# Optimization experiments

Measured on AMD Instinct MI355X. Metric: run time of the kernel, lower is better.

Reference implementation:

```python
import jax, jax.numpy as jnp
import numpy as np

B, N, NPOINT, NSAMPLE = 8, 8192, 2048, 64
RADIUS = 0.2
C_IN = 64  # input feature channels; mlp[0]=64 -> 67 after use_xyz concat


def setup_inputs() -> dict:
    key = jax.random.key(0)
    ks = jax.random.split(key, 12)
    xyz = jax.random.uniform(ks[0], (B, N, 3), dtype=jnp.float32)
    features = jax.random.normal(ks[1], (B, N, C_IN), dtype=jnp.float32)
    inds = jax.random.randint(ks[2], (B, NPOINT), 0, N, dtype=jnp.int32)

    def mkw(k, cin, cout):
        return jax.random.normal(k, (cin, cout), jnp.float32) * (1.0 / np.sqrt(cin).astype(np.float32))

    w0 = mkw(ks[3], C_IN + 3, 64)
    w1 = mkw(ks[4], 64, 64)
    w2 = mkw(ks[5], 64, 128)
    # BN (inference) folded into per-channel scale/shift
    s0 = 1.0 + 0.1 * jax.random.normal(ks[6], (64,), jnp.float32)
    t0 = 0.1 * jax.random.normal(ks[7], (64,), jnp.float32)
    s1 = 1.0 + 0.1 * jax.random.normal(ks[8], (64,), jnp.float32)
    t1 = 0.1 * jax.random.normal(ks[9], (64,), jnp.float32)
    s2 = 1.0 + 0.1 * jax.random.normal(ks[10], (128,), jnp.float32)
    t2 = 0.1 * jax.random.normal(ks[11], (128,), jnp.float32)
    return dict(xyz=xyz, features=features, inds=inds,
                w0=w0, s0=s0, t0=t0, w1=w1, s1=s1, t1=t1, w2=w2, s2=s2, t2=t2)


def _ball_query(xyz, new_xyz):
    """First NSAMPLE point indices within RADIUS of each query; pad by repeating
    the first hit (matches CUDA ball_query semantics). xyz:(B,N,3) new_xyz:(B,S,3)."""
    nn = jnp.sum(xyz * xyz, axis=-1)            # (B,N)
    qq = jnp.sum(new_xyz * new_xyz, axis=-1)    # (B,S)
    d2 = qq[:, :, None] + nn[:, None, :] - 2.0 * jnp.einsum('bsc,bnc->bsn', new_xyz, xyz)
    within = d2 < (RADIUS * RADIUS)
    ar = jnp.arange(N, dtype=jnp.int32)
    keyed = jnp.where(within, ar[None, None, :], N)   # out-of-radius -> sentinel N
    keyed = jnp.sort(keyed, axis=-1)[:, :, :NSAMPLE]  # first hits in point order
    idx = jnp.where(keyed == N, keyed[:, :, :1], keyed)
    return jnp.minimum(idx, N - 1)


_gather = jax.vmap(lambda pts, i: pts[i])  # (N,C),(M,) -> (M,C) per batch


def reference(xyz, features, inds, w0, s0, t0, w1, s1, t1, w2, s2, t2):
    new_xyz = _gather(xyz, inds)                              # (B,S,3)
    idx = _ball_query(xyz, new_xyz)                           # (B,S,ns)
    flat = idx.reshape(B, NPOINT * NSAMPLE)
    g_xyz = _gather(xyz, flat).reshape(B, NPOINT, NSAMPLE, 3)
    g_xyz = (g_xyz - new_xyz[:, :, None, :]) / RADIUS         # normalize_xyz
    g_feat = _gather(features, flat).reshape(B, NPOINT, NSAMPLE, C_IN)
    x = jnp.concatenate([g_xyz, g_feat], axis=-1)             # (B,S,ns,C+3)
    for wgt, s, t in ((w0, s0, t0), (w1, s1, t1), (w2, s2, t2)):
        x = jax.nn.relu(jnp.einsum('bpsc,cd->bpsd', x, wgt) * s + t)
    new_features = jnp.max(x, axis=2)                         # max-pool over nsample
    return new_xyz, new_features, inds, idx
```

## Files before the change

### kernel.cpp

```cpp
#include <hip/hip_runtime.h>

#define BB 8
#define NN 8192
#define NPOINT 2048
#define NSAMPLE 64
#define CIN 64
#define RADIUS 0.2f
#define R2 (RADIUS * RADIUS)

#define OFF_NEWXYZ 0
#define OFF_FEAT (BB * NPOINT * 3)
#define OFF_INDS (OFF_FEAT + BB * NPOINT * 128)
#define OFF_IDX (OFF_INDS + BB * NPOINT)

typedef _Float16 half8 __attribute__((ext_vector_type(8)));
typedef _Float16 half4 __attribute__((ext_vector_type(4)));
typedef __fp16 f16x2 __attribute__((ext_vector_type(2)));
typedef float floatx16 __attribute__((ext_vector_type(16)));

#define P0 88
#define P1 72
#define X_LOC 0
#define H_LOC (64 * P0)
#define XH_WAVE (64 * P0 + 64 * P1)
#define WT0_S 0
#define WT1_S (64 * P0)
#define WT2_S (64 * P0 + 64 * P1)

#define QPW 8

__global__ __launch_bounds__(256) void ballq_kernel(
    const float* __restrict__ xyz, const int* __restrict__ inds,
    float* __restrict__ out) {
  __shared__ int sidx[4][2][NSAMPLE];
  const int wave = (blockIdx.x * 256 + threadIdx.x) >> 6;
  const int lane = threadIdx.x & 63;
  const int wid = threadIdx.x >> 6;
  const int q0 = wave * 2, q1 = q0 + 1;
  const int b = q0 >> 11;

  const float* xb = xyz + (size_t)b * NN * 3;
  const int i0 = inds[q0], i1 = inds[q1];
  const float c0x = xb[i0 * 3 + 0], c0y = xb[i0 * 3 + 1], c0z = xb[i0 * 3 + 2];
  const float c1x = xb[i1 * 3 + 0], c1y = xb[i1 * 3 + 1], c1z = xb[i1 * 3 + 2];

  if (lane < 2) {
    const int qq_ = lane ? q1 : q0;
    const int ii = lane ? i1 : i0;
    out[OFF_NEWXYZ + (size_t)qq_ * 3 + 0] = lane ? c1x : c0x;
    out[OFF_NEWXYZ + (size_t)qq_ * 3 + 1] = lane ? c1y : c0y;
    out[OFF_NEWXYZ + (size_t)qq_ * 3 + 2] = lane ? c1z : c0z;
    out[OFF_INDS + qq_] = (float)ii;
  }

  const float qq0 = c0x * c0x + c0y * c0y + c0z * c0z;
  const float qq1 = c1x * c1x + c1y * c1y + c1z * c1z;

  int cnt0 = 0, cnt1 = 0;
  float ax[4], ay[4], az[4];
#pragma unroll
  for (int k = 0; k < 4; ++k) {
    const float* p = xb + (size_t)(k * 64 + lane) * 3;
    ax[k] = p[0];
    ay[k] = p[1];
    az[k] = p[2];
  }
  for (int j0 = 0; j0 < NN; j0 += 256) {
    float bx[4] = {0}, by[4] = {0}, bz[4] = {0};
    const int jn = j0 + 256;
    if (jn < NN) {
#pragma unroll
      for (int k = 0; k < 4; ++k) {
        const float* p = xb + (size_t)(jn + k * 64 + lane) * 3;
        bx[k] = p[0];
        by[k] = p[1];
        bz[k] = p[2];
      }
    }
#pragma unroll
    for (int k = 0; k < 4; ++k) {
      const int j = j0 + k * 64 + lane;
      const float nn_ = ax[k] * ax[k] + ay[k] * ay[k] + az[k] * az[k];
      const float dot0 = c0x * ax[k] + c0y * ay[k] + c0z * az[k];
      const float dot1 = c1x * ax[k] + c1y * ay[k] + c1z * az[k];
      const bool hit0 = (qq0 + nn_ - 2.0f * dot0) < R2;
      const bool hit1 = (qq1 + nn_ - 2.0f * dot1) < R2;
      const unsigned long long m0 = __ballot(hit0);
      const unsigned long long m1 = __ballot(hit1);
      if (hit0) {
        const int pos = cnt0 + (int)__popcll(m0 & ((1ull << lane) - 1ull));
        if (pos < NSAMPLE) sidx[wid][0][pos] = j;
      }
      if (hit1) {
        const int pos = cnt1 + (int)__popcll(m1 & ((1ull << lane) - 1ull));
        if (pos < NSAMPLE) sidx[wid][1][pos] = j;
      }
      cnt0 += (int)__popcll(m0);
      cnt1 += (int)__popcll(m1);
    }
    if (cnt0 >= NSAMPLE && cnt1 >= NSAMPLE) break;
#pragma unroll
    for (int k = 0; k < 4; ++k) {
      ax[k] = bx[k];
      ay[k] = by[k];
      az[k] = bz[k];
    }
  }
  const int v0 = sidx[wid][0][lane < cnt0 ? lane : 0];
  out[OFF_IDX + (size_t)q0 * NSAMPLE + lane] = (float)v0;
  const int v1 = sidx[wid][1][lane < cnt1 ? lane : 0];
  out[OFF_IDX + (size_t)q1 * NSAMPLE + lane] = (float)v1;
}

__global__ __launch_bounds__(128, 2) void mlp_mfma(
    const float* __restrict__ xyz, const float* __restrict__ features,
    const int* __restrict__ inds,
    const float* __restrict__ w0, const float* __restrict__ s0,
    const float* __restrict__ t0, const float* __restrict__ w1,
    const float* __restrict__ s1, const float* __restrict__ t1,
    const float* __restrict__ w2, const float* __restrict__ s2,
    const float* __restrict__ t2, float* __restrict__ out) {
  __shared__ _Float16 sm[2 * XH_WAVE];
  const int tid = threadIdx.x;
  const int w = tid >> 6;
  const int l = tid & 63;
  const int l31 = l & 31;
  const int h5 = l >> 5;
  const int koff = h5 * 8;

  {
    const int d = tid >> 1, hf = tid & 1;
    const float sd0 = s0[d], td0 = t0[d], sd1 = s1[d];
#pragma unroll
    for (int j = 0; j < 44; ++j) {
      const int c = hf * 44 + j;
      float v = 0.0f;
      if (c < 64) v = w0[(3 + c) * 64 + d] * sd0;
      else if (c < 67) v = w0[(c - 64) * 64 + d] * sd0;
      else if (c == 67) v = td0;
      sm[WT0_S + d * P0 + c] = (_Float16)v;
    }
#pragma unroll
    for (int j = 0; j < 32; ++j) {
      const int c = hf * 32 + j;
      sm[WT1_S + d * P1 + c] = (_Float16)(w1[c * 64 + d] * sd1);
    }
    const int ch = tid;
    const float sch = s2[ch];
#pragma unroll
    for (int c = 0; c < 64; ++c)
      sm[WT2_S + ch * P1 + c] = (_Float16)(w2[c * 128 + ch] * sch);
  }
  __syncthreads();

  half8 b0f[2][5], b1f[2][4], b2f[4][4];
#pragma unroll
  for (int nt = 0; nt < 2; ++nt)
#pragma unroll
    for (int ks = 0; ks < 5; ++ks)
      b0f[nt][ks] =
          *(const half8*)&sm[WT0_S + (nt * 32 + l31) * P0 + ks * 16 + koff];
#pragma unroll
  for (int nt = 0; nt < 2; ++nt)
#pragma unroll
    for (int ks = 0; ks < 4; ++ks)
      b1f[nt][ks] =
          *(const half8*)&sm[WT1_S + (nt * 32 + l31) * P1 + ks * 16 + koff];
#pragma unroll
  for (int ct = 0; ct < 4; ++ct)
#pragma unroll
    for (int ks = 0; ks < 4; ++ks)
      b2f[ct][ks] =
          *(const half8*)&sm[WT2_S + (ct * 32 + l31) * P1 + ks * 16 + koff];
  const float t1v0 = t1[l31];
  const float t1v1 = t1[32 + l31];
  float t2v[4];
#pragma unroll
  for (int ct = 0; ct < 4; ++ct) t2v[ct] = t2[ct * 32 + l31];
  __syncthreads();

  _Float16* xbuf = sm + w * XH_WAVE + X_LOC;
  _Float16* hbuf = sm + w * XH_WAVE + H_LOC;
  {
    half8 z = {};
    *(half8*)&xbuf[l * P0 + 72] = z;
  }

  const int wq0 = (blockIdx.x * 2 + w) * QPW;
  const int b = wq0 >> 11;
  const float* xb = xyz + (size_t)b * NN * 3;
  const float* fbase = features + (size_t)b * NN * CIN;

  int myidx = (int)out[OFF_IDX + (size_t)wq0 * NSAMPLE + l];
  int indv = inds[wq0];
  float cx = xb[indv * 3 + 0], cy = xb[indv * 3 + 1], cz = xb[indv * 3 + 2];
  float ppx = xb[myidx * 3 + 0], ppy = xb[myidx * 3 + 1],
        ppz = xb[myidx * 3 + 2];

#pragma unroll 1
  for (int qi = 0; qi < QPW; ++qi) {
    const int q = wq0 + qi;
    const int nq = (qi + 1 < QPW) ? q + 1 : q;

    float4 g[16];
#pragma unroll
    for (int i = 0; i < 16; ++i) {
      const int s = (l >> 2) + 16 * (i & 3);
      const int c = (l & 3) + 4 * (i >> 2);
      const int sidx = __shfl(myidx, s, 64);
      g[i] = *(const float4*)(fbase + (size_t)sidx * CIN + 4 * c);
    }
    const float fni = out[OFF_IDX + (size_t)nq * NSAMPLE + l];
    const int nindv = inds[nq];

#pragma unroll
    for (int i = 0; i < 16; ++i) {
      const int s = (l >> 2) + 16 * (i & 3);
      const int c = (l & 3) + 4 * (i >> 2);
      union {
        half4 v;
        f16x2 p[2];
      } hv;
      hv.p[0] = __builtin_amdgcn_cvt_pkrtz(g[i].x, g[i].y);
      hv.p[1] = __builtin_amdgcn_cvt_pkrtz(g[i].z, g[i].w);
      *(half4*)&xbuf[s * P0 + 4 * c] = hv.v;
    }
    {
      union {
        half8 v;
        f16x2 p[4];
      } xv;
      xv.p[0] =
          __builtin_amdgcn_cvt_pkrtz((ppx - cx) * 5.0f, (ppy - cy) * 5.0f);
      xv.p[1] = __builtin_amdgcn_cvt_pkrtz((ppz - cz) * 5.0f, 1.0f);
      xv.p[2] = __builtin_amdgcn_cvt_pkrtz(0.0f, 0.0f);
      xv.p[3] = __builtin_amdgcn_cvt_pkrtz(0.0f, 0.0f);
      *(half8*)&xbuf[l * P0 + 64] = xv.v;
    }

    {
      half8 xa[2][5];
#pragma unroll
      for (int st = 0; st < 2; ++st)
#pragma unroll
        for (int ks = 0; ks < 5; ++ks)
          xa[st][ks] =
              *(const half8*)&xbuf[(st * 32 + l31) * P0 + ks * 16 + koff];
#pragma unroll
      for (int nt = 0; nt < 2; ++nt)
#pragma unroll
        for (int st = 0; st < 2; ++st) {
          floatx16 acc;
#pragma unroll
          for (int i = 0; i < 16; ++i) acc[i] = 0.0f;
#pragma unroll
          for (int ks = 0; ks < 5; ++ks)
            acc = __builtin_amdgcn_mfma_f32_32x32x16_f16(xa[st][ks],
                                                         b0f[nt][ks], acc,
                                                         0, 0, 0);
#pragma unroll
          for (int reg = 0; reg < 16; ++reg) {
            const int row = st * 32 + (reg & 3) + 8 * (reg >> 2) + 4 * h5;
            hbuf[row * P1 + nt * 32 + l31] = (_Float16)fmaxf(acc[reg], 0.0f);
          }
        }
    }

    const int nidxs = (int)fni;
    const float ncx = xb[nindv * 3 + 0];
    const float ncy = xb[nindv * 3 + 1];
    const float ncz = xb[nindv * 3 + 2];
    const float nppx = xb[nidxs * 3 + 0];
    const float nppy = xb[nidxs * 3 + 1];
    const float nppz = xb[nidxs * 3 + 2];

    {
      half8 ha[2][4];
#pragma unroll
      for (int st = 0; st < 2; ++st)
#pragma unroll
        for (int ks = 0; ks < 4; ++ks)
          ha[st][ks] =
              *(const half8*)&hbuf[(st * 32 + l31) * P1 + ks * 16 + koff];
#pragma unroll
      for (int nt = 0; nt < 2; ++nt) {
        const float tt = nt ? t1v1 : t1v0;
#pragma unroll
        for (int st = 0; st < 2; ++st) {
          floatx16 acc;
#pragma unroll
          for (int i = 0; i < 16; ++i) acc[i] = 0.0f;
#pragma unroll
          for (int ks = 0; ks < 4; ++ks)
            acc = __builtin_amdgcn_mfma_f32_32x32x16_f16(ha[st][ks],
                                                         b1f[nt][ks], acc,
                                                         0, 0, 0);
#pragma unroll
          for (int reg = 0; reg < 16; ++reg) {
            const int row = st * 32 + (reg & 3) + 8 * (reg >> 2) + 4 * h5;
            xbuf[row * P0 + nt * 32 + l31] =
                (_Float16)fmaxf(acc[reg] + tt, 0.0f);
          }
        }
      }
    }

    {
      half8 h1a[2][4];
#pragma unroll
      for (int st = 0; st < 2; ++st)
#pragma unroll
        for (int ks = 0; ks < 4; ++ks)
          h1a[st][ks] =
              *(const half8*)&xbuf[(st * 32 + l31) * P0 + ks * 16 + koff];
#pragma unroll
      for (int ct = 0; ct < 4; ++ct) {
        floatx16 aA, aB;
#pragma unroll
        for (int i = 0; i < 16; ++i) {
          aA[i] = 0.0f;
          aB[i] = 0.0f;
        }
#pragma unroll
        for (int ks = 0; ks < 4; ++ks) {
          aA = __builtin_amdgcn_mfma_f32_32x32x16_f16(h1a[0][ks], b2f[ct][ks],
                                                      aA, 0, 0, 0);
          aB = __builtin_amdgcn_mfma_f32_32x32x16_f16(h1a[1][ks], b2f[ct][ks],
                                                      aB, 0, 0, 0);
        }
        float m = fmaxf(aA[0], aB[0]);
#pragma unroll
        for (int i = 1; i < 16; ++i) m = fmaxf(m, fmaxf(aA[i], aB[i]));
        float v = fmaxf(m + t2v[ct], 0.0f);
        v = fmaxf(v, __shfl_xor(v, 32, 64));
        if (l < 32) out[OFF_FEAT + (size_t)q * 128 + ct * 32 + l] = v;
      }
    }

    myidx = nidxs;
    cx = ncx; cy = ncy; cz = ncz;
    ppx = nppx; ppy = nppy; ppz = nppz;
  }
}

extern "C" void kernel_launch(void* const* d_in, const int* in_sizes, int n_in,
                              void* d_out, int out_size, void* d_ws,
                              size_t ws_size, hipStream_t stream) {
  const float* xyz = (const float*)d_in[0];
  const float* features = (const float*)d_in[1];
  const int* inds = (const int*)d_in[2];
  const float* w0 = (const float*)d_in[3];
  const float* s0 = (const float*)d_in[4];
  const float* t0 = (const float*)d_in[5];
  const float* w1 = (const float*)d_in[6];
  const float* s1 = (const float*)d_in[7];
  const float* t1 = (const float*)d_in[8];
  const float* w2 = (const float*)d_in[9];
  const float* s2 = (const float*)d_in[10];
  const float* t2 = (const float*)d_in[11];
  float* out = (float*)d_out;

  const int nquery = BB * NPOINT;
  ballq_kernel<<<nquery / 8, 256, 0, stream>>>(xyz, inds, out);
  mlp_mfma<<<nquery / (2 * QPW), 128, 0, stream>>>(
      xyz, features, inds, w0, s0, t0, w1, s1, t1, w2, s2, t2, out);
}
```

Before: 175.9 us.

## Pre-convert features to fp16 in workspace and swizzle MLP block order

The ball-query kernel now also converts the full feature tensor to fp16 in the workspace, one half8 per thread. The MLP kernel then gathers 16-byte half8 rows instead of float4 fp32 rows, which halves the gather traffic and removes the per-query conversion. Block indices are also permuted so consecutive blocks land on different batches, which may spread load across XCDs and caches. The cost is an extra full read of features and a write of the fp16 copy. The fp16 path is used only when the workspace is large enough, otherwise the old path runs.

```diff
diff --git a/kernel.cpp b/kernel.cpp
--- a/kernel.cpp
+++ b/kernel.cpp
@@ -31,7 +31,24 @@
 
 __global__ __launch_bounds__(256) void ballq_kernel(
     const float* __restrict__ xyz, const int* __restrict__ inds,
-    float* __restrict__ out) {
+    float* __restrict__ out, const float* __restrict__ features,
+    _Float16* __restrict__ f16f) {
+  if (f16f) {
+    const int t = blockIdx.x * 256 + threadIdx.x;
+    const float4* src = (const float4*)features;
+    const float4 a = src[2 * t + 0];
+    const float4 b = src[2 * t + 1];
+    union {
+      half8 v;
+      f16x2 p[4];
+    } u;
+    u.p[0] = __builtin_amdgcn_cvt_pkrtz(a.x, a.y);
+    u.p[1] = __builtin_amdgcn_cvt_pkrtz(a.z, a.w);
+    u.p[2] = __builtin_amdgcn_cvt_pkrtz(b.x, b.y);
+    u.p[3] = __builtin_amdgcn_cvt_pkrtz(b.z, b.w);
+    ((half8*)f16f)[t] = u.v;
+  }
+
   __shared__ int sidx[4][2][NSAMPLE];
   const int wave = (blockIdx.x * 256 + threadIdx.x) >> 6;
   const int lane = threadIdx.x & 63;
@@ -112,9 +129,10 @@
   out[OFF_IDX + (size_t)q1 * NSAMPLE + lane] = (float)v1;
 }
 
+template <bool F16>
 __global__ __launch_bounds__(128, 2) void mlp_mfma(
     const float* __restrict__ xyz, const float* __restrict__ features,
-    const int* __restrict__ inds,
+    const _Float16* __restrict__ f16f, const int* __restrict__ inds,
     const float* __restrict__ w0, const float* __restrict__ s0,
     const float* __restrict__ t0, const float* __restrict__ w1,
     const float* __restrict__ s1, const float* __restrict__ t1,
@@ -186,10 +204,12 @@
     *(half8*)&xbuf[l * P0 + 72] = z;
   }
 
-  const int wq0 = (blockIdx.x * 2 + w) * QPW;
+  const int lb = (blockIdx.x & 7) * ((int)gridDim.x >> 3) + (blockIdx.x >> 3);
+  const int wq0 = (lb * 2 + w) * QPW;
   const int b = wq0 >> 11;
   const float* xb = xyz + (size_t)b * NN * 3;
   const float* fbase = features + (size_t)b * NN * CIN;
+  const _Float16* fb16 = f16f + (size_t)b * NN * CIN;
 
   int myidx = (int)out[OFF_IDX + (size_t)wq0 * NSAMPLE + l];
   int indv = inds[wq0];
@@ -203,27 +223,45 @@
     const int nq = (qi + 1 < QPW) ? q + 1 : q;
 
     float4 g[16];
-#pragma unroll
-    for (int i = 0; i < 16; ++i) {
-      const int s = (l >> 2) + 16 * (i & 3);
-      const int c = (l & 3) + 4 * (i >> 2);
-      const int sidx = __shfl(myidx, s, 64);
-      g[i] = *(const float4*)(fbase + (size_t)sidx * CIN + 4 * c);
+    half8 gh[8];
+    if constexpr (F16) {
+#pragma unroll
+      for (int i = 0; i < 8; ++i) {
+        const int r = (l >> 3) + 8 * i;
+        const int sidx = __shfl(myidx, r, 64);
+        gh[i] = *(const half8*)(fb16 + (size_t)sidx * CIN + (l & 7) * 8);
+      }
+    } else {
+#pragma unroll
+      for (int i = 0; i < 16; ++i) {
+        const int s = (l >> 2) + 16 * (i & 3);
+        const int c = (l & 3) + 4 * (i >> 2);
+        const int sidx = __shfl(myidx, s, 64);
+        g[i] = *(const float4*)(fbase + (size_t)sidx * CIN + 4 * c);
+      }
     }
     const float fni = out[OFF_IDX + (size_t)nq * NSAMPLE + l];
     const int nindv = inds[nq];
 
-#pragma unroll
-    for (int i = 0; i < 16; ++i) {
-      const int s = (l >> 2) + 16 * (i & 3);
-      const int c = (l & 3) + 4 * (i >> 2);
-      union {
-        half4 v;
-        f16x2 p[2];
-      } hv;
-      hv.p[0] = __builtin_amdgcn_cvt_pkrtz(g[i].x, g[i].y);
-      hv.p[1] = __builtin_amdgcn_cvt_pkrtz(g[i].z, g[i].w);
-      *(half4*)&xbuf[s * P0 + 4 * c] = hv.v;
+    if constexpr (F16) {
+#pragma unroll
+      for (int i = 0; i < 8; ++i) {
+        const int r = (l >> 3) + 8 * i;
+        *(half8*)&xbuf[r * P0 + (l & 7) * 8] = gh[i];
+      }
+    } else {
+#pragma unroll
+      for (int i = 0; i < 16; ++i) {
+        const int s = (l >> 2) + 16 * (i & 3);
+        const int c = (l & 3) + 4 * (i >> 2);
+        union {
+          half4 v;
+          f16x2 p[2];
+        } hv;
+        hv.p[0] = __builtin_amdgcn_cvt_pkrtz(g[i].x, g[i].y);
+        hv.p[1] = __builtin_amdgcn_cvt_pkrtz(g[i].z, g[i].w);
+        *(half4*)&xbuf[s * P0 + 4 * c] = hv.v;
+      }
     }
     {
       union {
@@ -360,8 +398,15 @@
   const float* t2 = (const float*)d_in[11];
   float* out = (float*)d_out;
 
+  const size_t f16need = (size_t)BB * NN * CIN * sizeof(_Float16);
+  _Float16* f16f = (ws_size >= f16need) ? (_Float16*)d_ws : nullptr;
+
   const int nquery = BB * NPOINT;
-  ballq_kernel<<<nquery / 8, 256, 0, stream>>>(xyz, inds, out);
-  mlp_mfma<<<nquery / (2 * QPW), 128, 0, stream>>>(
-      xyz, features, inds, w0, s0, t0, w1, s1, t1, w2, s2, t2, out);
+  ballq_kernel<<<nquery / 8, 256, 0, stream>>>(xyz, inds, out, features, f16f);
+  if (f16f)
+    mlp_mfma<true><<<nquery / (2 * QPW), 128, 0, stream>>>(
+        xyz, features, f16f, inds, w0, s0, t0, w1, s1, t1, w2, s2, t2, out);
+  else
+    mlp_mfma<false><<<nquery / (2 * QPW), 128, 0, stream>>>(
+        xyz, features, f16f, inds, w0, s0, t0, w1, s1, t1, w2, s2, t2, out);
 }
```

Result: no change. 175.5 us (-0.2%).

## Keep MLP intermediate activations in registers via transposed MFMA and permlane32 swaps

Applied to the files above, without the earlier changes.

The first two MLP layers now compute the transposed product (weights as A operand) so each accumulator can be repacked into the next layer's input fragments with permlane32_swap, instead of going through LDS. The layer-1 bias is folded into an extra MFMA against a constant bias fragment, and the per-wave hidden buffer in shared memory is dropped, shrinking LDS use. Block indices are also remapped across the grid so neighbouring blocks land in different batches. This removes LDS stores, loads and waits between layers but adds cross-lane swap instructions and one extra MFMA per tile, and it raises register pressure.

```diff
diff --git a/kernel.cpp b/kernel.cpp
--- a/kernel.cpp
+++ b/kernel.cpp
@@ -17,15 +17,15 @@
 typedef _Float16 half4 __attribute__((ext_vector_type(4)));
 typedef __fp16 f16x2 __attribute__((ext_vector_type(2)));
 typedef float floatx16 __attribute__((ext_vector_type(16)));
+typedef unsigned int uint2v __attribute__((ext_vector_type(2)));
 
 #define P0 88
 #define P1 72
-#define X_LOC 0
-#define H_LOC (64 * P0)
-#define XH_WAVE (64 * P0 + 64 * P1)
 #define WT0_S 0
 #define WT1_S (64 * P0)
-#define WT2_S (64 * P0 + 64 * P1)
+#define WT2_S (WT1_S + 64 * P0)
+#define SM_H (WT2_S + 128 * P1)
+#define XSL (64 * P0)
 
 #define QPW 8
 
@@ -112,7 +112,36 @@
   out[OFF_IDX + (size_t)q1 * NSAMPLE + lane] = (float)v1;
 }
 
-__global__ __launch_bounds__(128, 2) void mlp_mfma(
+__device__ inline unsigned int pkru(float a, float b) {
+  union {
+    f16x2 p;
+    unsigned int u;
+  } t;
+  t.p = __builtin_amdgcn_cvt_pkrtz(fmaxf(a, 0.0f), fmaxf(b, 0.0f));
+  return t.u;
+}
+__device__ inline void build_frags(const floatx16& acc, half8& f0, half8& f1) {
+  unsigned int P[4], Q[4];
+#pragma unroll
+  for (int rg = 0; rg < 4; ++rg) {
+    P[rg] = pkru(acc[4 * rg + 0], acc[4 * rg + 1]);
+    Q[rg] = pkru(acc[4 * rg + 2], acc[4 * rg + 3]);
+  }
+  union {
+    unsigned int u[4];
+    half8 h;
+  } o;
+  uint2v sp = __builtin_amdgcn_permlane32_swap(P[0], P[1], false, false);
+  uint2v sq = __builtin_amdgcn_permlane32_swap(Q[0], Q[1], false, false);
+  o.u[0] = sp.x; o.u[1] = sq.x; o.u[2] = sp.y; o.u[3] = sq.y;
+  f0 = o.h;
+  sp = __builtin_amdgcn_permlane32_swap(P[2], P[3], false, false);
+  sq = __builtin_amdgcn_permlane32_swap(Q[2], Q[3], false, false);
+  o.u[0] = sp.x; o.u[1] = sq.x; o.u[2] = sp.y; o.u[3] = sq.y;
+  f1 = o.h;
+}
+
+__global__ __launch_bounds__(128, 2) void mlp_r(
     const float* __restrict__ xyz, const float* __restrict__ features,
     const int* __restrict__ inds,
     const float* __restrict__ w0, const float* __restrict__ s0,
@@ -120,7 +149,7 @@
     const float* __restrict__ s1, const float* __restrict__ t1,
     const float* __restrict__ w2, const float* __restrict__ s2,
     const float* __restrict__ t2, float* __restrict__ out) {
-  __shared__ _Float16 sm[2 * XH_WAVE];
+  __shared__ _Float16 sm[SM_H];
   const int tid = threadIdx.x;
   const int w = tid >> 6;
   const int l = tid & 63;
@@ -130,7 +159,7 @@
 
   {
     const int d = tid >> 1, hf = tid & 1;
-    const float sd0 = s0[d], td0 = t0[d], sd1 = s1[d];
+    const float sd0 = s0[d], td0 = t0[d], sd1 = s1[d], td1 = t1[d];
 #pragma unroll
     for (int j = 0; j < 44; ++j) {
       const int c = hf * 44 + j;
@@ -139,11 +168,10 @@
       else if (c < 67) v = w0[(c - 64) * 64 + d] * sd0;
       else if (c == 67) v = td0;
       sm[WT0_S + d * P0 + c] = (_Float16)v;
-    }
-#pragma unroll
-    for (int j = 0; j < 32; ++j) {
-      const int c = hf * 32 + j;
-      sm[WT1_S + d * P1 + c] = (_Float16)(w1[c * 64 + d] * sd1);
+      float v1 = 0.0f;
+      if (c < 64) v1 = w1[c * 64 + d] * sd1;
+      else if (c == 67) v1 = td1;
+      sm[WT1_S + d * P0 + c] = (_Float16)v1;
     }
     const int ch = tid;
     const float sch = s2[ch];
@@ -153,40 +181,38 @@
   }
   __syncthreads();
 
-  half8 b0f[2][5], b1f[2][4], b2f[4][4];
+  half8 b0f[2][5], b1f[2][5], b2f[4][4];
 #pragma unroll
   for (int nt = 0; nt < 2; ++nt)
 #pragma unroll
-    for (int ks = 0; ks < 5; ++ks)
+    for (int ks = 0; ks < 5; ++ks) {
       b0f[nt][ks] =
           *(const half8*)&sm[WT0_S + (nt * 32 + l31) * P0 + ks * 16 + koff];
-#pragma unroll
-  for (int nt = 0; nt < 2; ++nt)
-#pragma unroll
-    for (int ks = 0; ks < 4; ++ks)
       b1f[nt][ks] =
-          *(const half8*)&sm[WT1_S + (nt * 32 + l31) * P1 + ks * 16 + koff];
+          *(const half8*)&sm[WT1_S + (nt * 32 + l31) * P0 + ks * 16 + koff];
+    }
 #pragma unroll
   for (int ct = 0; ct < 4; ++ct)
 #pragma unroll
     for (int ks = 0; ks < 4; ++ks)
       b2f[ct][ks] =
           *(const half8*)&sm[WT2_S + (ct * 32 + l31) * P1 + ks * 16 + koff];
-  const float t1v0 = t1[l31];
-  const float t1v1 = t1[32 + l31];
   float t2v[4];
 #pragma unroll
   for (int ct = 0; ct < 4; ++ct) t2v[ct] = t2[ct * 32 + l31];
   __syncthreads();
 
-  _Float16* xbuf = sm + w * XH_WAVE + X_LOC;
-  _Float16* hbuf = sm + w * XH_WAVE + H_LOC;
+  half8 bias_f = {};
+  if (h5 == 0) bias_f[3] = (_Float16)1.0f;
+
+  _Float16* xbuf = sm + w * XSL;
   {
     half8 z = {};
     *(half8*)&xbuf[l * P0 + 72] = z;
   }
 
-  const int wq0 = (blockIdx.x * 2 + w) * QPW;
+  const int lb = (blockIdx.x & 7) * ((int)gridDim.x >> 3) + (blockIdx.x >> 3);
+  const int wq0 = (lb * 2 + w) * QPW;
   const int b = wq0 >> 11;
   const float* xb = xyz + (size_t)b * NN * 3;
   const float* fbase = features + (size_t)b * NN * CIN;
@@ -238,6 +264,7 @@
       *(half8*)&xbuf[l * P0 + 64] = xv.v;
     }
 
+    half8 xa1[2][4];
     {
       half8 xa[2][5];
 #pragma unroll
@@ -255,14 +282,10 @@
           for (int i = 0; i < 16; ++i) acc[i] = 0.0f;
 #pragma unroll
           for (int ks = 0; ks < 5; ++ks)
-            acc = __builtin_amdgcn_mfma_f32_32x32x16_f16(xa[st][ks],
-                                                         b0f[nt][ks], acc,
+            acc = __builtin_amdgcn_mfma_f32_32x32x16_f16(b0f[nt][ks],
+                                                         xa[st][ks], acc,
                                                          0, 0, 0);
-#pragma unroll
-          for (int reg = 0; reg < 16; ++reg) {
-            const int row = st * 32 + (reg & 3) + 8 * (reg >> 2) + 4 * h5;
-            hbuf[row * P1 + nt * 32 + l31] = (_Float16)fmaxf(acc[reg], 0.0f);
-          }
+          build_frags(acc, xa1[st][2 * nt], xa1[st][2 * nt + 1]);
         }
     }
 
@@ -274,17 +297,10 @@
     const float nppy = xb[nidxs * 3 + 1];
     const float nppz = xb[nidxs * 3 + 2];
 
+    half8 h1a[2][4];
     {
-      half8 ha[2][4];
-#pragma unroll
-      for (int st = 0; st < 2; ++st)
-#pragma unroll
-        for (int ks = 0; ks < 4; ++ks)
-          ha[st][ks] =
-              *(const half8*)&hbuf[(st * 32 + l31) * P1 + ks * 16 + koff];
-#pragma unroll
-      for (int nt = 0; nt < 2; ++nt) {
-        const float tt = nt ? t1v1 : t1v0;
+#pragma unroll
+      for (int nt = 0; nt < 2; ++nt)
 #pragma unroll
         for (int st = 0; st < 2; ++st) {
           floatx16 acc;
@@ -292,27 +308,16 @@
           for (int i = 0; i < 16; ++i) acc[i] = 0.0f;
 #pragma unroll
           for (int ks = 0; ks < 4; ++ks)
-            acc = __builtin_amdgcn_mfma_f32_32x32x16_f16(ha[st][ks],
-                                                         b1f[nt][ks], acc,
+            acc = __builtin_amdgcn_mfma_f32_32x32x16_f16(b1f[nt][ks],
+                                                         xa1[st][ks], acc,
                                                          0, 0, 0);
-#pragma unroll
-          for (int reg = 0; reg < 16; ++reg) {
-            const int row = st * 32 + (reg & 3) + 8 * (reg >> 2) + 4 * h5;
-            xbuf[row * P0 + nt * 32 + l31] =
-                (_Float16)fmaxf(acc[reg] + tt, 0.0f);
-          }
+          acc = __builtin_amdgcn_mfma_f32_32x32x16_f16(b1f[nt][4], bias_f,
+                                                       acc, 0, 0, 0);
+          build_frags(acc, h1a[st][2 * nt], h1a[st][2 * nt + 1]);
         }
-      }
     }
 
     {
-      half8 h1a[2][4];
-#pragma unroll
-      for (int st = 0; st < 2; ++st)
-#pragma unroll
-        for (int ks = 0; ks < 4; ++ks)
-          h1a[st][ks] =
-              *(const half8*)&xbuf[(st * 32 + l31) * P0 + ks * 16 + koff];
 #pragma unroll
       for (int ct = 0; ct < 4; ++ct) {
         floatx16 aA, aB;
@@ -362,6 +367,6 @@
 
   const int nquery = BB * NPOINT;
   ballq_kernel<<<nquery / 8, 256, 0, stream>>>(xyz, inds, out);
-  mlp_mfma<<<nquery / (2 * QPW), 128, 0, stream>>>(
+  mlp_r<<<nquery / (2 * QPW), 128, 0, stream>>>(
       xyz, features, inds, w0, s0, t0, w1, s1, t1, w2, s2, t2, out);
 }
```

Result: no change. 175.0 us (-0.5%).
